# Performance work log

Measured on AMD Instinct MI355X. Metric: run time of the kernel, lower is better.

The kernel has to match this reference:

```python
import math
import jax, jax.numpy as jnp
import numpy as np

B, T, C, H = 4, 2048, 1024, 16

def _rope_cos_sin(dim, max_pos):
    half = dim // 2
    pos = jnp.arange(max_pos, dtype=jnp.float32)[:, None]
    freqs = jnp.exp(jnp.arange(half, dtype=jnp.float32) * (-math.log(10000.0) / (half - 1)))[None, :]
    args = pos * freqs  # [T, half]
    return jnp.cos(args), jnp.sin(args)

def _apply_rope(x, cos, sin):
    # x: [B, H, T, D]; pairs (even, odd) along D form complex numbers
    xr = x[..., 0::2]
    xi = x[..., 1::2]
    c = cos[None, None, :, :]
    s = sin[None, None, :, :]
    out_r = xr * c - xi * s
    out_i = xr * s + xi * c
    return jnp.stack([out_r, out_i], axis=-1).reshape(x.shape)

def setup_inputs() -> dict:
    key = jax.random.key(0)
    ks = jax.random.split(key, 9)
    sc = 1.0 / math.sqrt(C)
    return {
        "x": jax.random.normal(ks[0], (B, T, C), jnp.float32),
        "Wq": jax.random.normal(ks[1], (C, C), jnp.float32) * sc,
        "bq": jax.random.normal(ks[2], (C,), jnp.float32) * 0.01,
        "Wk": jax.random.normal(ks[3], (C, C), jnp.float32) * sc,
        "bk": jax.random.normal(ks[4], (C,), jnp.float32) * 0.01,
        "Wv": jax.random.normal(ks[5], (C, C), jnp.float32) * sc,
        "bv": jax.random.normal(ks[6], (C,), jnp.float32) * 0.01,
        "Wp": jax.random.normal(ks[7], (C, C), jnp.float32) * sc,
        "bp": jax.random.normal(ks[8], (C,), jnp.float32) * 0.01,
        "n_head": H,
    }

def reference(x, Wq, bq, Wk, bk, Wv, bv, Wp, bp, n_head):
    Bx, Tx, Cx = x.shape
    D = Cx // n_head
    def heads(w, b):
        return (x @ w + b).reshape(Bx, Tx, n_head, D).transpose(0, 2, 1, 3)  # [B,H,T,D]
    q = heads(Wq, bq)
    k = heads(Wk, bk)
    v = heads(Wv, bv)
    cos, sin = _rope_cos_sin(D, Tx)
    q = _apply_rope(q, cos, sin)
    k = _apply_rope(k, cos, sin)
    att = jnp.einsum("bhtd,bhsd->bhts", q, k) * (1.0 / math.sqrt(D))
    causal = jnp.tril(jnp.ones((Tx, Tx), dtype=bool))
    att = jnp.where(causal[None, None, :, :], att, jnp.float32(-1e10))
    att = jax.nn.softmax(att, axis=-1)
    y = jnp.einsum("bhts,bhsd->bhtd", att, v)
    y = y.transpose(0, 2, 1, 3).reshape(Bx, Tx, Cx)
    return y @ Wp + bp
```

## Files before the change

kernel.cpp:

```cpp
#include <hip/hip_runtime.h>
#include <hip/hip_bf16.h>
#include <stdint.h>

namespace {

constexpr int Bx = 4, Tx = 2048, Cx = 1024, Hx = 16, Dx = 64;
constexpr int Mx = Bx * Tx;

typedef __attribute__((ext_vector_type(8))) short bf16x8;
typedef __attribute__((ext_vector_type(4))) float f32x4;
typedef __attribute__((ext_vector_type(16))) float f32x16;
typedef __attribute__((ext_vector_type(2))) unsigned int u32x2;

__device__ __forceinline__ float b2f(unsigned short u) {
  unsigned int v = ((unsigned int)u) << 16;
  return __builtin_bit_cast(float, v);
}
__device__ __forceinline__ unsigned short f2b(float f) {
  unsigned int v = __builtin_bit_cast(unsigned int, f);
  v += 0x7fffu + ((v >> 16) & 1u);
  return (unsigned short)(v >> 16);
}
__device__ __forceinline__ uint32_t pkbf(float a, float b) {
  __hip_bfloat162 h = __float22bfloat162_rn(float2{a, b});
  uint32_t r;
  __builtin_memcpy(&r, &h, 4);
  return r;
}
__device__ __forceinline__ void pl32swap(uint32_t& a, uint32_t& b) {
  u32x2 r = __builtin_amdgcn_permlane32_swap(a, b, false, false);
  a = r[0];
  b = r[1];
}

#define GLD16(g, lp) __builtin_amdgcn_global_load_lds(                     \
    (__attribute__((address_space(1))) void*)(g),                          \
    (__attribute__((address_space(3))) void*)(lp), 16, 0, 0)

__global__ void ca_cvt(const float* __restrict__ src, unsigned short* __restrict__ dst, int n4) {
  int i = blockIdx.x * blockDim.x + threadIdx.x;
  int stride = gridDim.x * blockDim.x;
  for (; i < n4; i += stride) {
    float4 f = ((const float4*)src)[i];
    ushort4 o;
    o.x = f2b(f.x); o.y = f2b(f.y); o.z = f2b(f.z); o.w = f2b(f.w);
    ((ushort4*)dst)[i] = o;
  }
}

__global__ void ca_wt(const float* __restrict__ W, unsigned short* __restrict__ Wt) {
  __shared__ float tile[32][33];
  int n0 = blockIdx.x * 32, k0 = blockIdx.y * 32;
  int j = threadIdx.x & 31, i = threadIdx.x >> 5;
#pragma unroll
  for (int r = 0; r < 4; ++r)
    tile[i + 8 * r][j] = W[(size_t)(k0 + i + 8 * r) * Cx + n0 + j];
  __syncthreads();
#pragma unroll
  for (int r = 0; r < 4; ++r)
    Wt[(size_t)(n0 + i + 8 * r) * Cx + k0 + j] = f2b(tile[j][i + 8 * r]);
}

__global__ void ca_rtab(float* __restrict__ ct, float* __restrict__ st) {
  int idx = blockIdx.x * blockDim.x + threadIdx.x;
  int t = idx >> 5, i = idx & 31;
  float fr = expf((float)i * -0.29710775393471563f);
  float a = (float)t * fr;
  ct[idx] = cosf(a);
  st[idx] = sinf(a);
}

template <int MODE>
__global__ __launch_bounds__(256) void ca_gemm(
    const unsigned short* __restrict__ A, const unsigned short* __restrict__ Bt,
    const float* __restrict__ b0, const float* __restrict__ b1, const float* __restrict__ b2,
    const float* __restrict__ ctab, const float* __restrict__ stab,
    void* __restrict__ out, int M, int N, int K) {
  __shared__ __align__(16) unsigned short Al[128 * 32];
  __shared__ __align__(16) unsigned short Bl[128 * 32];
  int tid = threadIdx.x;
  int w = tid >> 6, l = tid & 63;
  int m0 = blockIdx.x * 128, n0 = blockIdx.y * 128;
  int wm = (w >> 1) * 64, wn = (w & 1) * 64;
  f32x4 acc[4][4] = {};

  int lr = l & 15, lk8 = (l >> 4) * 8;
  int srow = w * 32 + (l >> 2), scol = (l & 3) * 8;
  const unsigned short* ga0 = A + (size_t)(m0 + srow) * K + scol;
  const unsigned short* gb0 = Bt + (size_t)(n0 + srow) * K + scol;
  unsigned short* la = &Al[w * 1024];
  unsigned short* lb = &Bl[w * 1024];
  int nk = K / 32;
  for (int kt = 0; kt < nk; ++kt) {
    const unsigned short* ga = ga0 + kt * 32;
    const unsigned short* gb = gb0 + kt * 32;
    GLD16(ga, la);
    GLD16(ga + (size_t)16 * K, la + 512);
    GLD16(gb, lb);
    GLD16(gb + (size_t)16 * K, lb + 512);
    __syncthreads();
    bf16x8 af[4], bfr[4];
#pragma unroll
    for (int mi = 0; mi < 4; ++mi) af[mi] = *(const bf16x8*)&Al[(wm + mi * 16 + lr) * 32 + lk8];
#pragma unroll
    for (int ni = 0; ni < 4; ++ni) bfr[ni] = *(const bf16x8*)&Bl[(wn + ni * 16 + lr) * 32 + lk8];
#pragma unroll
    for (int mi = 0; mi < 4; ++mi)
#pragma unroll
      for (int ni = 0; ni < 4; ++ni)
        acc[mi][ni] = __builtin_amdgcn_mfma_f32_16x16x32_bf16(af[mi], bfr[ni], acc[mi][ni], 0, 0, 0);
    __syncthreads();
  }

  int lq4 = (l >> 4) * 4;
  if (MODE == 0) {
    constexpr float SC = 0.18033688011112042f;
    int which = n0 >> 10;
    int nb = n0 & 1023;
    const float* bias = which == 0 ? b0 : (which == 1 ? b1 : b2);
    unsigned short* o = (unsigned short*)out + (size_t)which * M * 1024;
    bool doRope = which < 2;
    float scl = which == 0 ? SC : 1.0f;
#pragma unroll
    for (int mi = 0; mi < 4; ++mi)
#pragma unroll
      for (int ni = 0; ni < 4; ++ni) {
        int ncol = nb + wn + ni * 16 + lr;
        float bv = bias[ncol];
        int j = (ncol & 63) >> 1;
        bool even = (ncol & 1) == 0;
#pragma unroll
        for (int rg = 0; rg < 4; ++rg) {
          int m = m0 + wm + mi * 16 + lq4 + rg;
          float val = acc[mi][ni][rg] + bv;
          if (doRope) {
            int t = m & (Tx - 1);
            float c = ctab[t * 32 + j], s = stab[t * 32 + j];
            float other = __shfl_xor(val, 1);
            float res = even ? (val * c - other * s) : (other * s + val * c);
            val = res * scl;
          }
          o[(size_t)m * 1024 + ncol] = f2b(val);
        }
      }
  } else {
    float* o = (float*)out;
#pragma unroll
    for (int mi = 0; mi < 4; ++mi)
#pragma unroll
      for (int ni = 0; ni < 4; ++ni) {
        int ncol = n0 + wn + ni * 16 + lr;
        float bv = b0[ncol];
#pragma unroll
        for (int rg = 0; rg < 4; ++rg) {
          int m = m0 + wm + mi * 16 + lq4 + rg;
          o[(size_t)m * N + ncol] = acc[mi][ni][rg] + bv;
        }
      }
  }
}

__global__ void ca_vt(const unsigned short* __restrict__ v, unsigned short* __restrict__ vT) {
  __shared__ __align__(16) unsigned short tl[64][72];
  int t0 = blockIdx.x * 64;
  int bh = blockIdx.y;
  int b = bh >> 4, h = bh & 15;
  int tid = threadIdx.x;
  const unsigned short* vb = v + (size_t)b * Tx * Cx + h * Dx;
#pragma unroll
  for (int it = 0; it < 2; ++it) {
    int tt = it * 32 + (tid >> 3), d0 = (tid & 7) * 8;
    uint4 x = *(const uint4*)&vb[(size_t)(t0 + tt) * Cx + d0];
    unsigned short* u = (unsigned short*)&x;
#pragma unroll
    for (int jj = 0; jj < 8; ++jj) tl[d0 + jj][tt] = u[jj];
  }
  __syncthreads();
  unsigned short* o = vT + (size_t)bh * Dx * Tx;
#pragma unroll
  for (int it = 0; it < 2; ++it) {
    int d = it * 32 + (tid >> 3), tc = (tid & 7) * 8;
    *(uint4*)&o[(size_t)d * Tx + t0 + tc] = *(const uint4*)&tl[d][tc];
  }
}

__global__ __launch_bounds__(64) void ca_kvfl(
    const unsigned short* __restrict__ k, const unsigned short* __restrict__ vT,
    unsigned short* __restrict__ kfl, unsigned short* __restrict__ vfl) {
  int l = threadIdx.x & 63;
  int bh = blockIdx.x, t = blockIdx.y;
  int b = bh >> 4, h = bh & 15;
  int lo = l & 31, hi = l >> 5;
  const unsigned short* kr = k + (size_t)b * Tx * Cx + h * Dx + (size_t)(t * 32 + lo) * Cx + hi * 8;
  const unsigned short* vr = vT + (size_t)bh * Dx * Tx + (size_t)lo * Tx + t * 32 + hi * 8;
  unsigned short* ko = kfl + ((size_t)bh * 64 + t) * 2048;
  unsigned short* vo = vfl + ((size_t)bh * 64 + t) * 2048;
#pragma unroll
  for (int c = 0; c < 4; ++c) {
    uint4 x = *(const uint4*)(kr + c * 16);
    *(uint4*)(ko + c * 512 + l * 8) = x;
  }
#pragma unroll
  for (int dc = 0; dc < 2; ++dc)
#pragma unroll
    for (int kc = 0; kc < 2; ++kc) {
      uint4 x = *(const uint4*)(vr + (size_t)dc * 32 * Tx + kc * 16);
      *(uint4*)(vo + (dc * 2 + kc) * 512 + l * 8) = x;
    }
}

__global__ __launch_bounds__(64) void ca_attn(
    const unsigned short* __restrict__ q, const unsigned short* __restrict__ kfl,
    const unsigned short* __restrict__ vfl, unsigned short* __restrict__ y) {
  __shared__ uint32_t els[32][33];
  int l = threadIdx.x & 63;
  int bh = blockIdx.x;
  int jp = (int)blockIdx.y;
  int b = bh >> 4, h16 = bh & 15;
  const unsigned short* qp = q + (size_t)b * Tx * Cx + h16 * Dx;
  const unsigned short* kb = kfl + (size_t)bh * 64 * 2048 + l * 8;
  const unsigned short* vb = vfl + (size_t)bh * 64 * 2048 + l * 8;
  int lo = l & 31, hi = l >> 5;
  constexpr float SHIFT = 20.0f;
  const uint32_t one2 = 0x3F803F80u;
  uint4 onesw{one2, one2, one2, one2};
  bf16x8 ONES = __builtin_bit_cast(bf16x8, onesw);

  for (int pass = 0; pass < 2; ++pass) {
    int qt = pass ? 63 - jp : jp;
    int qbase = qt * 32;

    bf16x8 qf[4];
    {
      const unsigned short* qr = qp + (size_t)(qbase + lo) * Cx + hi * 8;
#pragma unroll
      for (int c = 0; c < 4; ++c) qf[c] = *(const bf16x8*)(qr + c * 16);
    }

    f32x16 acc0 = {}, acc1 = {}, sacc = {};
    int nt = qt + 1;

    uint4 rk[4], rv[4];
    auto loadK = [&](int t) {
#pragma unroll
      for (int c = 0; c < 4; ++c) rk[c] = *(const uint4*)(kb + t * 2048 + c * 512);
    };
    auto loadV = [&](int t) {
#pragma unroll
      for (int j = 0; j < 4; ++j) rv[j] = *(const uint4*)(vb + t * 2048 + j * 512);
    };
    loadK(0);
    loadV(0);

    for (int t = 0; t < nt; ++t) {
      bf16x8 kf[4], vf[4];
#pragma unroll
      for (int c = 0; c < 4; ++c) kf[c] = __builtin_bit_cast(bf16x8, rk[c]);
#pragma unroll
      for (int c = 0; c < 4; ++c) vf[c] = __builtin_bit_cast(bf16x8, rv[c]);
      if (t + 1 < nt) { loadK(t + 1); loadV(t + 1); }

      __builtin_amdgcn_s_setprio(1);
      f32x16 s = {};
      s = __builtin_amdgcn_mfma_f32_32x32x16_bf16(kf[0], qf[0], s, 0, 0, 0);
      s = __builtin_amdgcn_mfma_f32_32x32x16_bf16(kf[1], qf[1], s, 0, 0, 0);
      s = __builtin_amdgcn_mfma_f32_32x32x16_bf16(kf[2], qf[2], s, 0, 0, 0);
      s = __builtin_amdgcn_mfma_f32_32x32x16_bf16(kf[3], qf[3], s, 0, 0, 0);
      __builtin_amdgcn_s_setprio(0);

      float p[16];
      if (t == nt - 1) {
#pragma unroll
        for (int r = 0; r < 16; ++r) {
          int kvr = (r & 3) + 8 * (r >> 2) + 4 * hi;
          p[r] = (kvr > lo) ? 0.f : exp2f(s[r] - SHIFT);
        }
      } else {
#pragma unroll
        for (int r = 0; r < 16; ++r) p[r] = exp2f(s[r] - SHIFT);
      }

      uint32_t pk[8];
#pragma unroll
      for (int i = 0; i < 8; ++i) pk[i] = pkbf(p[2 * i], p[2 * i + 1]);
      pl32swap(pk[0], pk[2]);
      pl32swap(pk[1], pk[3]);
      pl32swap(pk[4], pk[6]);
      pl32swap(pk[5], pk[7]);
      uint4 xw{pk[0], pk[1], pk[2], pk[3]}, yw{pk[4], pk[5], pk[6], pk[7]};
      bf16x8 PB0 = __builtin_bit_cast(bf16x8, xw);
      bf16x8 PB1 = __builtin_bit_cast(bf16x8, yw);
      __builtin_amdgcn_s_setprio(1);
      acc0 = __builtin_amdgcn_mfma_f32_32x32x16_bf16(vf[0], PB0, acc0, 0, 0, 0);
      acc1 = __builtin_amdgcn_mfma_f32_32x32x16_bf16(vf[2], PB0, acc1, 0, 0, 0);
      sacc = __builtin_amdgcn_mfma_f32_32x32x16_bf16(ONES, PB0, sacc, 0, 0, 0);
      acc0 = __builtin_amdgcn_mfma_f32_32x32x16_bf16(vf[1], PB1, acc0, 0, 0, 0);
      acc1 = __builtin_amdgcn_mfma_f32_32x32x16_bf16(vf[3], PB1, acc1, 0, 0, 0);
      sacc = __builtin_amdgcn_mfma_f32_32x32x16_bf16(ONES, PB1, sacc, 0, 0, 0);
      __builtin_amdgcn_s_setprio(0);
    }

    float rl = __builtin_amdgcn_rcpf(sacc[0]);
#pragma unroll
    for (int dc = 0; dc < 2; ++dc) {
      f32x16 a = dc ? acc1 : acc0;
#pragma unroll
      for (int i = 0; i < 8; ++i) {
        uint32_t pkd = pkbf(a[2 * i] * rl, a[2 * i + 1] * rl);
        int d2 = (i & 1) + 4 * (i >> 1) + 2 * hi + dc * 16;
        els[lo][d2] = pkd;
      }
    }
    __syncthreads();
    unsigned short* yp = y + (size_t)b * Tx * Cx + h16 * Dx;
#pragma unroll
    for (int pp = 0; pp < 16; ++pp) {
      int qr = 2 * pp + hi;
      uint32_t val = els[qr][lo];
      *(uint32_t*)(yp + (size_t)(qbase + qr) * Cx + lo * 2) = val;
    }
    __syncthreads();
  }
}

}

extern "C" void kernel_launch(void* const* d_in, const int* in_sizes, int n_in,
                              void* d_out, int out_size, void* d_ws, size_t ws_size,
                              hipStream_t stream) {
  const float* x = (const float*)d_in[0];
  const float* Wq = (const float*)d_in[1];
  const float* bq = (const float*)d_in[2];
  const float* Wk = (const float*)d_in[3];
  const float* bk = (const float*)d_in[4];
  const float* Wv = (const float*)d_in[5];
  const float* bv = (const float*)d_in[6];
  const float* Wp = (const float*)d_in[7];
  const float* bp = (const float*)d_in[8];

  unsigned short* xb = (unsigned short*)d_ws;
  unsigned short* wt = xb + (size_t)Mx * Cx;
  float* ct = (float*)(wt + (size_t)4 * Cx * Cx);
  float* st = ct + Tx * 32;
  unsigned short* qb = (unsigned short*)(st + Tx * 32);
  unsigned short* kb = qb + (size_t)Mx * Cx;
  unsigned short* vb = kb + (size_t)Mx * Cx;
  unsigned short* vT = vb + (size_t)Mx * Cx;
  unsigned short* yb = vT + (size_t)Mx * Cx;
  unsigned short* kfl = yb + (size_t)Mx * Cx;
  unsigned short* vfl = kfl + (size_t)64 * 64 * 2048;

  ca_cvt<<<dim3(2048), dim3(256), 0, stream>>>(x, xb, Mx * Cx / 4);
  ca_wt<<<dim3(32, 32), dim3(256), 0, stream>>>(Wq, wt + (size_t)0 * Cx * Cx);
  ca_wt<<<dim3(32, 32), dim3(256), 0, stream>>>(Wk, wt + (size_t)1 * Cx * Cx);
  ca_wt<<<dim3(32, 32), dim3(256), 0, stream>>>(Wv, wt + (size_t)2 * Cx * Cx);
  ca_wt<<<dim3(32, 32), dim3(256), 0, stream>>>(Wp, wt + (size_t)3 * Cx * Cx);
  ca_rtab<<<dim3(Tx * 32 / 256), dim3(256), 0, stream>>>(ct, st);

  ca_gemm<0><<<dim3(64, 24), dim3(256), 0, stream>>>(xb, wt, bq, bk, bv, ct, st, qb, Mx, 3072, Cx);
  ca_vt<<<dim3(Tx / 64, Bx * Hx), dim3(256), 0, stream>>>(vb, vT);
  ca_kvfl<<<dim3(64, 64), dim3(64), 0, stream>>>(kb, vT, kfl, vfl);
  ca_attn<<<dim3(64, 32), dim3(64), 0, stream>>>(qb, kfl, vfl, yb);
  ca_gemm<1><<<dim3(64, 8), dim3(256), 0, stream>>>(yb, wt + (size_t)3 * Cx * Cx, bp,
                                                    nullptr, nullptr, nullptr, nullptr,
                                                    d_out, Mx, Cx, Cx);
}
```

Measured before the change: 236.5 us.

## Double-buffer GEMM LDS tiles and fuse V transpose into fragment layout

```diff
diff --git a/kernel.cpp b/kernel.cpp
--- a/kernel.cpp
+++ b/kernel.cpp
@@ -76,8 +76,8 @@
     const float* __restrict__ b0, const float* __restrict__ b1, const float* __restrict__ b2,
     const float* __restrict__ ctab, const float* __restrict__ stab,
     void* __restrict__ out, int M, int N, int K) {
-  __shared__ __align__(16) unsigned short Al[128 * 32];
-  __shared__ __align__(16) unsigned short Bl[128 * 32];
+  __shared__ __align__(16) unsigned short Al[2][128 * 32];
+  __shared__ __align__(16) unsigned short Bl[2][128 * 32];
   int tid = threadIdx.x;
   int w = tid >> 6, l = tid & 63;
   int m0 = blockIdx.x * 128, n0 = blockIdx.y * 128;
@@ -88,28 +88,36 @@
   int srow = w * 32 + (l >> 2), scol = (l & 3) * 8;
   const unsigned short* ga0 = A + (size_t)(m0 + srow) * K + scol;
   const unsigned short* gb0 = Bt + (size_t)(n0 + srow) * K + scol;
-  unsigned short* la = &Al[w * 1024];
-  unsigned short* lb = &Bl[w * 1024];
   int nk = K / 32;
-  for (int kt = 0; kt < nk; ++kt) {
+  auto stage = [&](int kt, int buf) {
     const unsigned short* ga = ga0 + kt * 32;
     const unsigned short* gb = gb0 + kt * 32;
+    unsigned short* la = &Al[buf][w * 1024];
+    unsigned short* lb = &Bl[buf][w * 1024];
     GLD16(ga, la);
     GLD16(ga + (size_t)16 * K, la + 512);
     GLD16(gb, lb);
     GLD16(gb + (size_t)16 * K, lb + 512);
-    __syncthreads();
+  };
+  stage(0, 0);
+  __syncthreads();
+  int cur = 0;
+  for (int kt = 0; kt < nk; ++kt) {
+    if (kt + 1 < nk) stage(kt + 1, cur ^ 1);
     bf16x8 af[4], bfr[4];
 #pragma unroll
-    for (int mi = 0; mi < 4; ++mi) af[mi] = *(const bf16x8*)&Al[(wm + mi * 16 + lr) * 32 + lk8];
-#pragma unroll
-    for (int ni = 0; ni < 4; ++ni) bfr[ni] = *(const bf16x8*)&Bl[(wn + ni * 16 + lr) * 32 + lk8];
+    for (int mi = 0; mi < 4; ++mi)
+      af[mi] = *(const bf16x8*)&Al[cur][(wm + mi * 16 + lr) * 32 + lk8];
+#pragma unroll
+    for (int ni = 0; ni < 4; ++ni)
+      bfr[ni] = *(const bf16x8*)&Bl[cur][(wn + ni * 16 + lr) * 32 + lk8];
 #pragma unroll
     for (int mi = 0; mi < 4; ++mi)
 #pragma unroll
       for (int ni = 0; ni < 4; ++ni)
         acc[mi][ni] = __builtin_amdgcn_mfma_f32_16x16x32_bf16(af[mi], bfr[ni], acc[mi][ni], 0, 0, 0);
     __syncthreads();
+    cur ^= 1;
   }
 
   int lq4 = (l >> 4) * 4;
@@ -160,8 +168,8 @@
   }
 }
 
-__global__ void ca_vt(const unsigned short* __restrict__ v, unsigned short* __restrict__ vT) {
-  __shared__ __align__(16) unsigned short tl[64][72];
+__global__ void ca_vfl(const unsigned short* __restrict__ v, unsigned short* __restrict__ vfl) {
+  __shared__ __align__(16) unsigned short tl[64][80];
   int t0 = blockIdx.x * 64;
   int bh = blockIdx.y;
   int b = bh >> 4, h = bh & 15;
@@ -176,37 +184,31 @@
     for (int jj = 0; jj < 8; ++jj) tl[d0 + jj][tt] = u[jj];
   }
   __syncthreads();
-  unsigned short* o = vT + (size_t)bh * Dx * Tx;
-#pragma unroll
-  for (int it = 0; it < 2; ++it) {
-    int d = it * 32 + (tid >> 3), tc = (tid & 7) * 8;
-    *(uint4*)&o[(size_t)d * Tx + t0 + tc] = *(const uint4*)&tl[d][tc];
-  }
-}
-
-__global__ __launch_bounds__(64) void ca_kvfl(
-    const unsigned short* __restrict__ k, const unsigned short* __restrict__ vT,
-    unsigned short* __restrict__ kfl, unsigned short* __restrict__ vfl) {
+  int l = tid & 63, lo = l & 31, hi = l >> 5;
+  int g = tid >> 6, tloc = g >> 1, kc = g & 1;
+  int tglob = (t0 >> 5) + tloc;
+  unsigned short* vo = vfl + ((size_t)bh * 64 + tglob) * 2048;
+#pragma unroll
+  for (int dc = 0; dc < 2; ++dc) {
+    int j = dc * 2 + kc;
+    uint4 x = *(const uint4*)&tl[dc * 32 + lo][tloc * 32 + hi * 8 + kc * 16];
+    *(uint4*)(vo + j * 512 + l * 8) = x;
+  }
+}
+
+__global__ __launch_bounds__(64) void ca_kfl(
+    const unsigned short* __restrict__ k, unsigned short* __restrict__ kfl) {
   int l = threadIdx.x & 63;
   int bh = blockIdx.x, t = blockIdx.y;
   int b = bh >> 4, h = bh & 15;
   int lo = l & 31, hi = l >> 5;
   const unsigned short* kr = k + (size_t)b * Tx * Cx + h * Dx + (size_t)(t * 32 + lo) * Cx + hi * 8;
-  const unsigned short* vr = vT + (size_t)bh * Dx * Tx + (size_t)lo * Tx + t * 32 + hi * 8;
   unsigned short* ko = kfl + ((size_t)bh * 64 + t) * 2048;
-  unsigned short* vo = vfl + ((size_t)bh * 64 + t) * 2048;
 #pragma unroll
   for (int c = 0; c < 4; ++c) {
     uint4 x = *(const uint4*)(kr + c * 16);
     *(uint4*)(ko + c * 512 + l * 8) = x;
   }
-#pragma unroll
-  for (int dc = 0; dc < 2; ++dc)
-#pragma unroll
-    for (int kc = 0; kc < 2; ++kc) {
-      uint4 x = *(const uint4*)(vr + (size_t)dc * 32 * Tx + kc * 16);
-      *(uint4*)(vo + (dc * 2 + kc) * 512 + l * 8) = x;
-    }
 }
 
 __global__ __launch_bounds__(64) void ca_attn(
@@ -358,8 +360,8 @@
   ca_rtab<<<dim3(Tx * 32 / 256), dim3(256), 0, stream>>>(ct, st);
 
   ca_gemm<0><<<dim3(64, 24), dim3(256), 0, stream>>>(xb, wt, bq, bk, bv, ct, st, qb, Mx, 3072, Cx);
-  ca_vt<<<dim3(Tx / 64, Bx * Hx), dim3(256), 0, stream>>>(vb, vT);
-  ca_kvfl<<<dim3(64, 64), dim3(64), 0, stream>>>(kb, vT, kfl, vfl);
+  ca_vfl<<<dim3(Tx / 64, Bx * Hx), dim3(256), 0, stream>>>(vb, vfl);
+  ca_kfl<<<dim3(64, 64), dim3(64), 0, stream>>>(kb, kfl);
   ca_attn<<<dim3(64, 32), dim3(64), 0, stream>>>(qb, kfl, vfl, yb);
   ca_gemm<1><<<dim3(64, 8), dim3(256), 0, stream>>>(yb, wt + (size_t)3 * Cx * Cx, bp,
                                                     nullptr, nullptr, nullptr, nullptr,
```

Measured after the change: 224.5 us. -5.1%, faster.
